# Optimization experiments

Measured on AMD Instinct MI355X. Metric: run time of the kernel, lower is better.

## Reference

```python
import jax, jax.numpy as jnp
import numpy as np
import math

B, N = 1, 512
C_S, C_Z, C_H, H, PQ, PV = 384, 128, 16, 12, 4, 8
INF, EPS = 100000.0, 1e-8


def setup_inputs() -> dict:
    key = jax.random.key(0)
    ks = jax.random.split(key, 16)
    sc = 0.02
    return {
        "s": jax.random.normal(ks[0], (B, N, C_S), jnp.float32),
        "z": jax.random.normal(ks[1], (B, N, N, C_Z), jnp.float32),
        "t_trans": jax.random.normal(ks[2], (B, N, 3), jnp.float32),
        "t_rots": jax.random.normal(ks[3], (B, N, 3, 3), jnp.float32),
        "mask": jnp.ones((B, N), jnp.float32),
        "Wq": jax.random.normal(ks[4], (C_S, H * C_H), jnp.float32) * sc,
        "bq": jnp.zeros((H * C_H,), jnp.float32),
        "Wkv": jax.random.normal(ks[5], (C_S, 2 * H * C_H), jnp.float32) * sc,
        "bkv": jnp.zeros((2 * H * C_H,), jnp.float32),
        "Wqp": jax.random.normal(ks[6], (C_S, H * PQ * 3), jnp.float32) * sc,
        "bqp": jnp.zeros((H * PQ * 3,), jnp.float32),
        "Wkvp": jax.random.normal(ks[7], (C_S, H * (PQ + PV) * 3), jnp.float32) * sc,
        "bkvp": jnp.zeros((H * (PQ + PV) * 3,), jnp.float32),
        "Wb": jax.random.normal(ks[8], (C_Z, H), jnp.float32) * sc,
        "bb": jnp.zeros((H,), jnp.float32),
        "head_weights": jnp.full((H,), 0.5413, jnp.float32),  # softplus^-1(1) init
        "Wout": jax.random.normal(ks[9], (H * (C_Z + C_H + PV * 4), C_S), jnp.float32) * sc,
        "bout": jnp.zeros((C_S,), jnp.float32),
    }


def _split3_stack(x):
    # torch.split into 3 chunks along -1, then stack on new last axis -> [..., P, 3]
    return jnp.stack(jnp.split(x, 3, axis=-1), axis=-1)


def reference(s, z, t_trans, t_rots, mask, Wq, bq, Wkv, bkv, Wqp, bqp, Wkvp, bkvp,
              Wb, bb, head_weights, Wout, bout):
    q = (s @ Wq + bq).reshape(B, N, H, C_H)
    kv = (s @ Wkv + bkv).reshape(B, N, H, 2 * C_H)
    k, v = kv[..., :C_H], kv[..., C_H:]

    # point projections, moved to global frame: r @ p + t
    qp = _split3_stack(s @ Wqp + bqp)                      # [B,N,H*PQ,3] local
    qp = jnp.einsum('bnij,bnpj->bnpi', t_rots, qp) + t_trans[:, :, None, :]
    q_pts = qp.reshape(B, N, H, PQ, 3)
    kvp = _split3_stack(s @ Wkvp + bkvp)                   # [B,N,H*(PQ+PV),3]
    kvp = jnp.einsum('bnij,bnpj->bnpi', t_rots, kvp) + t_trans[:, :, None, :]
    kvp = kvp.reshape(B, N, H, PQ + PV, 3)
    k_pts, v_pts = kvp[..., :PQ, :], kvp[..., PQ:, :]

    b = z @ Wb + bb                                        # [B,N,N,H]

    a = jnp.einsum('bihc,bjhc->bhij', q, k) * math.sqrt(1.0 / (3 * C_H))
    a = a + math.sqrt(1.0 / 3) * jnp.transpose(b, (0, 3, 1, 2))

    # point-distance attention: [B,N,N,H,PQ]
    d2 = jnp.sum((q_pts[:, :, None] - k_pts[:, None]) ** 2, axis=-1)
    hw = jax.nn.softplus(head_weights) * math.sqrt(1.0 / (3 * (PQ * 9.0 / 2)))
    a = a + (-0.5) * jnp.einsum('bijhp,h->bhij', d2, hw)

    square_mask = INF * (mask[:, :, None] * mask[:, None, :] - 1.0)  # [B,N,N]
    a = jax.nn.softmax(a + square_mask[:, None], axis=-1)  # [B,H,N,N]

    o = jnp.einsum('bhij,bjhc->bihc', a, v).reshape(B, N, H * C_H)

    o_pt = jnp.einsum('bhij,bjhpx->bihpx', a, v_pts)       # [B,N,H,PV,3] global
    # invert frame: r^T @ (p - t)
    o_pt = jnp.einsum('bnji,bnhpj->bnhpi', t_rots, o_pt - t_trans[:, :, None, None, :])
    o_pt_norm = jnp.sqrt(jnp.sum(o_pt ** 2, axis=-1) + EPS).reshape(B, N, H * PV)
    o_pt = o_pt.reshape(B, N, H * PV, 3)

    o_pair = jnp.einsum('bhij,bijc->bihc', a, z).reshape(B, N, H * C_Z)

    cat = jnp.concatenate(
        [o, o_pt[..., 0], o_pt[..., 1], o_pt[..., 2], o_pt_norm, o_pair], axis=-1)
    return cat @ Wout + bout
```

## Files before the change

kernel.cpp:

```cpp
#include <hip/hip_runtime.h>
#include <math.h>

#define N 512
#define CS 384
#define CZ 128
#define CH 16
#define NH 12
#define PQ 4
#define PV 8

#define OFF_Q     0
#define OFF_K     98304
#define OFF_V     196608
#define OFF_QRAW  294912
#define OFF_KVRAW 368640
#define OFF_QPTS  589824
#define OFF_KPTS  663552
#define OFF_VPTS  737280
#define OFF_A     884736
#define OFF_CAT   4030464

__global__ __launch_bounds__(128) void proj_kernel(
    const float* __restrict__ s,
    const float* __restrict__ Wq,  const float* __restrict__ bq,
    const float* __restrict__ Wkv, const float* __restrict__ bkv,
    const float* __restrict__ Wqp, const float* __restrict__ bqp,
    const float* __restrict__ Wkvp,const float* __restrict__ bkvp,
    float* __restrict__ ws)
{
    __shared__ float st[16 * CS];
    const int n0 = blockIdx.x * 16;
    for (int idx = threadIdx.x * 4; idx < 16 * CS; idx += 128 * 4)
        *(float4*)&st[idx] = *(const float4*)&s[n0 * CS + idx];
    __syncthreads();

    const int tc = threadIdx.x & 31;
    const int tr = threadIdx.x >> 5;
    const int u0 = blockIdx.y * 128 + tc * 4;
    const int r0 = tr * 4;

    const float* W; const float* bptr; int ncol, lc0;
    if (u0 < 192)      { W = Wq;   bptr = bq;   ncol = 192; lc0 = u0; }
    else if (u0 < 576) { W = Wkv;  bptr = bkv;  ncol = 384; lc0 = u0 - 192; }
    else if (u0 < 720) { W = Wqp;  bptr = bqp;  ncol = 144; lc0 = u0 - 576; }
    else               { W = Wkvp; bptr = bkvp; ncol = 432; lc0 = u0 - 720; }

    float acc[4][4];
    #pragma unroll
    for (int r = 0; r < 4; r++)
        #pragma unroll
        for (int c = 0; c < 4; c++) acc[r][c] = 0.f;

    for (int k = 0; k < CS; k += 4) {
        float4 w0 = *(const float4*)&W[(k + 0) * ncol + lc0];
        float4 w1 = *(const float4*)&W[(k + 1) * ncol + lc0];
        float4 w2 = *(const float4*)&W[(k + 2) * ncol + lc0];
        float4 w3 = *(const float4*)&W[(k + 3) * ncol + lc0];
        #pragma unroll
        for (int r = 0; r < 4; r++) {
            float4 sv = *(const float4*)&st[(r0 + r) * CS + k];
            acc[r][0] += sv.x * w0.x + sv.y * w1.x + sv.z * w2.x + sv.w * w3.x;
            acc[r][1] += sv.x * w0.y + sv.y * w1.y + sv.z * w2.y + sv.w * w3.y;
            acc[r][2] += sv.x * w0.z + sv.y * w1.z + sv.z * w2.z + sv.w * w3.z;
            acc[r][3] += sv.x * w0.w + sv.y * w1.w + sv.z * w2.w + sv.w * w3.w;
        }
    }

    #pragma unroll
    for (int c = 0; c < 4; c++) {
        const int u = u0 + c;
        const float bias = bptr[lc0 + c];
        #pragma unroll
        for (int r = 0; r < 4; r++) {
            const int n = n0 + r0 + r;
            int oidx;
            if (u < 192) oidx = OFF_Q + n * 192 + u;
            else if (u < 576) {
                int lc = u - 192, h = lc >> 5, w = lc & 31;
                oidx = (w < 16) ? OFF_K + n * 192 + h * 16 + w
                                : OFF_V + n * 192 + h * 16 + (w - 16);
            } else if (u < 720) oidx = OFF_QRAW + n * 144 + (u - 576);
            else                oidx = OFF_KVRAW + n * 432 + (u - 720);
            ws[oidx] = acc[r][c] + bias;
        }
    }
}

__global__ __launch_bounds__(192) void point_kernel(
    const float* __restrict__ t_trans, const float* __restrict__ t_rots,
    float* __restrict__ ws)
{
    const int n = blockIdx.x;
    const int t = threadIdx.x;
    __shared__ float R[9], tr[3];
    if (t < 9) R[t] = t_rots[n * 9 + t];
    if (t < 3) tr[t] = t_trans[n * 3 + t];
    __syncthreads();

    float x0, x1, x2;
    int base;
    if (t < 48) {
        int idx = t;
        x0 = ws[OFF_QRAW + n * 144 + 0 * 48 + idx];
        x1 = ws[OFF_QRAW + n * 144 + 1 * 48 + idx];
        x2 = ws[OFF_QRAW + n * 144 + 2 * 48 + idx];
        int h = idx >> 2, p = idx & 3;
        base = OFF_QPTS + ((n * NH + h) * PQ + p) * 3;
    } else {
        int idx = t - 48;
        x0 = ws[OFF_KVRAW + n * 432 + 0 * 144 + idx];
        x1 = ws[OFF_KVRAW + n * 432 + 1 * 144 + idx];
        x2 = ws[OFF_KVRAW + n * 432 + 2 * 144 + idx];
        int h = idx / 12, p = idx % 12;
        if (p < PQ) base = OFF_KPTS + ((n * NH + h) * PQ + p) * 3;
        else        base = OFF_VPTS + ((n * NH + h) * PV + (p - PQ)) * 3;
    }
    ws[base + 0] = R[0] * x0 + R[1] * x1 + R[2] * x2 + tr[0];
    ws[base + 1] = R[3] * x0 + R[4] * x1 + R[5] * x2 + tr[1];
    ws[base + 2] = R[6] * x0 + R[7] * x1 + R[8] * x2 + tr[2];
}

__global__ __launch_bounds__(192) void logitA_kernel(
    const float* __restrict__ mask, const float* __restrict__ hweights,
    float* __restrict__ ws)
{
    const int j0 = blockIdx.x * 16;
    const int i0 = blockIdx.y * 16;
    const int t = threadIdx.x;

    __shared__ float qt[16 * 200];
    __shared__ float kt[16 * 200];
    __shared__ float qpt[16 * 148];
    __shared__ float kpt[16 * 148];
    __shared__ float mi[16], mj[16];

    {
        const float* src = ws + OFF_Q + i0 * 192;
        for (int idx = t * 4; idx < 3072; idx += 768) {
            float4 v = *(const float4*)&src[idx];
            *(float4*)&qt[(idx / 192) * 200 + idx % 192] = v;
        }
    }
    {
        const float* src = ws + OFF_K + j0 * 192;
        for (int idx = t * 4; idx < 3072; idx += 768) {
            float4 v = *(const float4*)&src[idx];
            *(float4*)&kt[(idx / 192) * 200 + idx % 192] = v;
        }
    }
    {
        const float* src = ws + OFF_QPTS + i0 * 144;
        for (int idx = t * 4; idx < 2304; idx += 768) {
            float4 v = *(const float4*)&src[idx];
            *(float4*)&qpt[(idx / 144) * 148 + idx % 144] = v;
        }
    }
    {
        const float* src = ws + OFF_KPTS + j0 * 144;
        for (int idx = t * 4; idx < 2304; idx += 768) {
            float4 v = *(const float4*)&src[idx];
            *(float4*)&kpt[(idx / 144) * 148 + idx % 144] = v;
        }
    }
    if (t < 16) { mi[t] = mask[i0 + t]; mj[t] = mask[j0 + t]; }
    __syncthreads();

    const int jj = t & 15;
    const int h = t >> 4;
    const float hw = log1pf(expf(hweights[h])) * 0.13608276348795434f;
    const float cqk = 0.14433756729740643f;

    float4 kr0 = *(const float4*)&kt[jj * 200 + h * 16 + 0];
    float4 kr1 = *(const float4*)&kt[jj * 200 + h * 16 + 4];
    float4 kr2 = *(const float4*)&kt[jj * 200 + h * 16 + 8];
    float4 kr3 = *(const float4*)&kt[jj * 200 + h * 16 + 12];
    float4 kp0 = *(const float4*)&kpt[jj * 148 + h * 12 + 0];
    float4 kp1 = *(const float4*)&kpt[jj * 148 + h * 12 + 4];
    float4 kp2 = *(const float4*)&kpt[jj * 148 + h * 12 + 8];
    const float mjv = mj[jj];

    for (int ii = 0; ii < 16; ii++) {
        float4 q0 = *(const float4*)&qt[ii * 200 + h * 16 + 0];
        float4 q1 = *(const float4*)&qt[ii * 200 + h * 16 + 4];
        float4 q2 = *(const float4*)&qt[ii * 200 + h * 16 + 8];
        float4 q3 = *(const float4*)&qt[ii * 200 + h * 16 + 12];
        float qk = q0.x * kr0.x + q0.y * kr0.y + q0.z * kr0.z + q0.w * kr0.w
                 + q1.x * kr1.x + q1.y * kr1.y + q1.z * kr1.z + q1.w * kr1.w
                 + q2.x * kr2.x + q2.y * kr2.y + q2.z * kr2.z + q2.w * kr2.w
                 + q3.x * kr3.x + q3.y * kr3.y + q3.z * kr3.z + q3.w * kr3.w;
        float4 p0 = *(const float4*)&qpt[ii * 148 + h * 12 + 0];
        float4 p1 = *(const float4*)&qpt[ii * 148 + h * 12 + 4];
        float4 p2 = *(const float4*)&qpt[ii * 148 + h * 12 + 8];
        float e, d2 = 0.f;
        e = p0.x - kp0.x; d2 += e * e;  e = p0.y - kp0.y; d2 += e * e;
        e = p0.z - kp0.z; d2 += e * e;  e = p0.w - kp0.w; d2 += e * e;
        e = p1.x - kp1.x; d2 += e * e;  e = p1.y - kp1.y; d2 += e * e;
        e = p1.z - kp1.z; d2 += e * e;  e = p1.w - kp1.w; d2 += e * e;
        e = p2.x - kp2.x; d2 += e * e;  e = p2.y - kp2.y; d2 += e * e;
        e = p2.z - kp2.z; d2 += e * e;  e = p2.w - kp2.w; d2 += e * e;
        float sm = 100000.0f * (mi[ii] * mjv - 1.0f);
        ws[OFF_A + ((size_t)(i0 + ii) * NH + h) * N + j0 + jj] =
            qk * cqk - 0.5f * hw * d2 + sm;
    }
}

__global__ __launch_bounds__(512) void bsoft_kernel(
    const float* __restrict__ z, const float* __restrict__ Wb,
    const float* __restrict__ bb, float* __restrict__ ws)
{
    const int i = blockIdx.x;
    const int t = threadIdx.x;
    __shared__ float zt[128 * 132];
    __shared__ float wbt[12 * 132];
    __shared__ float wred[8][4];

    for (int idx = t; idx < CZ * NH; idx += 512) {
        int c = idx / NH, h = idx % NH;
        wbt[h * 132 + c] = Wb[idx];
    }

    const int jj = t & 127;
    const int hg = t >> 7;
    const int h0 = hg * 3;
    const float bb0 = bb[h0], bb1 = bb[h0 + 1], bb2 = bb[h0 + 2];
    const float cb = 0.5773502691896258f;

    float lg[3][4];

    for (int T = 0; T < 4; T++) {
        __syncthreads();
        const float* zsrc = z + ((size_t)i * N + T * 128) * CZ;
        for (int idx = t * 4; idx < 16384; idx += 2048) {
            float4 v = *(const float4*)&zsrc[idx];
            *(float4*)&zt[(idx >> 7) * 132 + (idx & 127)] = v;
        }
        __syncthreads();

        float a0 = bb0, a1 = bb1, a2 = bb2;
        const float* zr = &zt[jj * 132];
        const float* w0 = &wbt[(h0 + 0) * 132];
        const float* w1 = &wbt[(h0 + 1) * 132];
        const float* w2 = &wbt[(h0 + 2) * 132];
        #pragma unroll
        for (int c = 0; c < CZ; c += 4) {
            float4 zq = *(const float4*)&zr[c];
            float4 q0 = *(const float4*)&w0[c];
            float4 q1 = *(const float4*)&w1[c];
            float4 q2 = *(const float4*)&w2[c];
            a0 += zq.x * q0.x + zq.y * q0.y + zq.z * q0.z + zq.w * q0.w;
            a1 += zq.x * q1.x + zq.y * q1.y + zq.z * q1.z + zq.w * q1.w;
            a2 += zq.x * q2.x + zq.y * q2.y + zq.z * q2.z + zq.w * q2.w;
        }
        const float* arow = ws + OFF_A + (size_t)i * NH * N + T * 128 + jj;
        lg[0][T] = arow[(size_t)(h0 + 0) * N] + cb * a0;
        lg[1][T] = arow[(size_t)(h0 + 1) * N] + cb * a1;
        lg[2][T] = arow[(size_t)(h0 + 2) * N] + cb * a2;
    }

    const int wv = t >> 6;
    float mx[3], sm[3];
    #pragma unroll
    for (int r = 0; r < 3; r++) {
        float m = fmaxf(fmaxf(lg[r][0], lg[r][1]), fmaxf(lg[r][2], lg[r][3]));
        #pragma unroll
        for (int o = 32; o > 0; o >>= 1) m = fmaxf(m, __shfl_xor(m, o));
        mx[r] = m;
    }
    if ((t & 63) == 0) {
        wred[wv][0] = mx[0]; wred[wv][1] = mx[1]; wred[wv][2] = mx[2];
    }
    __syncthreads();
    #pragma unroll
    for (int r = 0; r < 3; r++)
        mx[r] = fmaxf(wred[hg * 2][r], wred[hg * 2 + 1][r]);
    __syncthreads();
    #pragma unroll
    for (int r = 0; r < 3; r++) {
        float s = 0.f;
        #pragma unroll
        for (int T = 0; T < 4; T++) { lg[r][T] = __expf(lg[r][T] - mx[r]); s += lg[r][T]; }
        #pragma unroll
        for (int o = 32; o > 0; o >>= 1) s += __shfl_xor(s, o);
        sm[r] = s;
    }
    if ((t & 63) == 0) {
        wred[wv][0] = sm[0]; wred[wv][1] = sm[1]; wred[wv][2] = sm[2];
    }
    __syncthreads();
    #pragma unroll
    for (int r = 0; r < 3; r++) {
        float inv = 1.0f / (wred[hg * 2][r] + wred[hg * 2 + 1][r]);
        float* prow = ws + OFF_A + ((size_t)i * NH + h0 + r) * N + jj;
        #pragma unroll
        for (int T = 0; T < 4; T++)
            prow[T * 128] = lg[r][T] * inv;
    }
}

__global__ __launch_bounds__(832) void finish_kernel(
    const float* __restrict__ z, const float* __restrict__ t_trans,
    const float* __restrict__ t_rots, const float* __restrict__ ws_c,
    float* __restrict__ ws)
{
    const int i = blockIdx.x;
    const int t = threadIdx.x;
    __shared__ float a_s[12 * 520];

    {
        const float* src = ws_c + OFF_A + (size_t)i * (NH * N);
        for (int idx = t * 4; idx < NH * N; idx += 832 * 4) {
            float4 v = *(const float4*)&src[idx];
            int h = idx >> 9, j = idx & 511;
            *(float4*)&a_s[h * 520 + j] = v;
        }
    }
    __syncthreads();

    float* cat = ws + OFF_CAT + (size_t)i * 2112;

    if (t < 512) {
        const int c = t & 127, hg = t >> 7;
        const float* zrow = z + (size_t)i * N * CZ + c;
        const float* a0 = a_s + (hg + 0) * 520;
        const float* a1 = a_s + (hg + 4) * 520;
        const float* a2 = a_s + (hg + 8) * 520;
        float acc0 = 0.f, acc1 = 0.f, acc2 = 0.f;
        #pragma unroll 8
        for (int j = 0; j < N; j++) {
            float zv = zrow[(size_t)j * CZ];
            acc0 += a0[j] * zv; acc1 += a1[j] * zv; acc2 += a2[j] * zv;
        }
        cat[576 + (hg + 0) * CZ + c] = acc0;
        cat[576 + (hg + 4) * CZ + c] = acc1;
        cat[576 + (hg + 8) * CZ + c] = acc2;
    } else if (t < 704) {
        const int u = t - 512, h = u >> 4, cc = u & 15;
        const float* vcol = ws_c + OFF_V + h * 16 + cc;
        const float* ah = a_s + h * 520;
        float acc = 0.f;
        #pragma unroll 8
        for (int j = 0; j < N; j++)
            acc += ah[j] * vcol[j * 192];
        cat[h * 16 + cc] = acc;
    } else if (t < 800) {
        const int u = t - 704, h = u >> 3, p = u & 7;
        const float* vp = ws_c + OFF_VPTS + (h * PV + p) * 3;
        const float* ah = a_s + h * 520;
        float g0 = 0.f, g1 = 0.f, g2 = 0.f;
        #pragma unroll 4
        for (int j = 0; j < N; j++) {
            float av = ah[j];
            const float* vpj = vp + j * (NH * PV * 3);
            g0 += av * vpj[0]; g1 += av * vpj[1]; g2 += av * vpj[2];
        }
        float R[9], ti[3];
        #pragma unroll
        for (int x = 0; x < 9; x++) R[x] = t_rots[i * 9 + x];
        #pragma unroll
        for (int x = 0; x < 3; x++) ti[x] = t_trans[i * 3 + x];
        g0 -= ti[0]; g1 -= ti[1]; g2 -= ti[2];
        float l0 = R[0] * g0 + R[3] * g1 + R[6] * g2;
        float l1 = R[1] * g0 + R[4] * g1 + R[7] * g2;
        float l2 = R[2] * g0 + R[5] * g1 + R[8] * g2;
        float nrm = sqrtf(l0 * l0 + l1 * l1 + l2 * l2 + 1e-8f);
        int e = h * PV + p;
        cat[192 + e] = l0;
        cat[288 + e] = l1;
        cat[384 + e] = l2;
        cat[480 + e] = nrm;
    }
}

__global__ __launch_bounds__(384) void init_out_kernel(
    const float* __restrict__ bout, float* __restrict__ out)
{
    out[(size_t)blockIdx.x * 384 + threadIdx.x] = bout[threadIdx.x];
}

__global__ __launch_bounds__(384) void out_kernel(
    const float* __restrict__ Wout, const float* __restrict__ ws,
    float* __restrict__ out)
{
    const int rt = blockIdx.x;
    const int kc = blockIdx.y;
    const int t = threadIdx.x;
    __shared__ float ct[16 * 264];
    for (int idx = t * 4; idx < 16 * 264; idx += 384 * 4) {
        int rr = idx / 264, kk = idx % 264;
        *(float4*)&ct[idx] =
            *(const float4*)&ws[OFF_CAT + (size_t)(rt * 16 + rr) * 2112 + kc * 264 + kk];
    }
    __syncthreads();
    const int cq = t % 96, rg = t / 96;
    const int c0 = cq * 4;
    float acc[4][4] = {};
    const float* Wp = Wout + (size_t)kc * 264 * 384 + c0;
    for (int kk = 0; kk < 264; kk++) {
        float4 w = *(const float4*)&Wp[(size_t)kk * 384];
        #pragma unroll
        for (int r = 0; r < 4; r++) {
            float sv = ct[(rg * 4 + r) * 264 + kk];
            acc[r][0] += sv * w.x; acc[r][1] += sv * w.y;
            acc[r][2] += sv * w.z; acc[r][3] += sv * w.w;
        }
    }
    #pragma unroll
    for (int r = 0; r < 4; r++) {
        float* op = out + (size_t)(rt * 16 + rg * 4 + r) * 384 + c0;
        atomicAdd(&op[0], acc[r][0]);
        atomicAdd(&op[1], acc[r][1]);
        atomicAdd(&op[2], acc[r][2]);
        atomicAdd(&op[3], acc[r][3]);
    }
}

extern "C" void kernel_launch(void* const* d_in, const int* in_sizes, int n_in,
                              void* d_out, int out_size, void* d_ws, size_t ws_size,
                              hipStream_t stream) {
    const float* s       = (const float*)d_in[0];
    const float* z       = (const float*)d_in[1];
    const float* t_trans = (const float*)d_in[2];
    const float* t_rots  = (const float*)d_in[3];
    const float* mask    = (const float*)d_in[4];
    const float* Wq      = (const float*)d_in[5];
    const float* bq      = (const float*)d_in[6];
    const float* Wkv     = (const float*)d_in[7];
    const float* bkv     = (const float*)d_in[8];
    const float* Wqp     = (const float*)d_in[9];
    const float* bqp     = (const float*)d_in[10];
    const float* Wkvp    = (const float*)d_in[11];
    const float* bkvp    = (const float*)d_in[12];
    const float* Wb      = (const float*)d_in[13];
    const float* bb      = (const float*)d_in[14];
    const float* hweights= (const float*)d_in[15];
    const float* Wout    = (const float*)d_in[16];
    const float* bout    = (const float*)d_in[17];
    float* ws  = (float*)d_ws;
    float* out = (float*)d_out;

    init_out_kernel<<<512, 384, 0, stream>>>(bout, out);
    proj_kernel<<<dim3(32, 9), 128, 0, stream>>>(s, Wq, bq, Wkv, bkv, Wqp, bqp, Wkvp, bkvp, ws);
    point_kernel<<<512, 192, 0, stream>>>(t_trans, t_rots, ws);
    logitA_kernel<<<dim3(32, 32), 192, 0, stream>>>(mask, hweights, ws);
    bsoft_kernel<<<512, 512, 0, stream>>>(z, Wb, bb, ws);
    finish_kernel<<<512, 832, 0, stream>>>(z, t_trans, t_rots, ws, ws);
    out_kernel<<<dim3(32, 8), 384, 0, stream>>>(Wout, ws, out);
}
```

Measured before the change: 427.5 us.

## Retile finish, bsoft, proj and out kernels with vectorized loads and planar v-points

Several kernels change at once. finish_kernel drops from 832 to 384 threads: each thread now computes a float4 of channels for two heads in the z pair reduction, and the o and point reductions use float4 loads over j. v_pts is stored as planar x/y/z arrays indexed by position so the point reduction can read it contiguously. bsoft reads Wb through scalar, wave-uniform loads instead of staging it in shared memory, proj_kernel doubles its thread count with fewer rows per thread, and out_kernel unrolls k by 4 with float4 shared-memory reads. The aim is fewer scalar loads and better memory coalescing, at the cost of more registers per thread and a __syncthreads inside the j loop of finish_kernel.

```diff
diff --git a/kernel.cpp b/kernel.cpp
--- a/kernel.cpp
+++ b/kernel.cpp
@@ -17,10 +17,11 @@
 #define OFF_QPTS  589824
 #define OFF_KPTS  663552
 #define OFF_VPTS  737280
+#define VPLANE    49152
 #define OFF_A     884736
 #define OFF_CAT   4030464
 
-__global__ __launch_bounds__(128) void proj_kernel(
+__global__ __launch_bounds__(256) void proj_kernel(
     const float* __restrict__ s,
     const float* __restrict__ Wq,  const float* __restrict__ bq,
     const float* __restrict__ Wkv, const float* __restrict__ bkv,
@@ -30,14 +31,14 @@
 {
     __shared__ float st[16 * CS];
     const int n0 = blockIdx.x * 16;
-    for (int idx = threadIdx.x * 4; idx < 16 * CS; idx += 128 * 4)
+    for (int idx = threadIdx.x * 4; idx < 16 * CS; idx += 256 * 4)
         *(float4*)&st[idx] = *(const float4*)&s[n0 * CS + idx];
     __syncthreads();
 
     const int tc = threadIdx.x & 31;
     const int tr = threadIdx.x >> 5;
     const int u0 = blockIdx.y * 128 + tc * 4;
-    const int r0 = tr * 4;
+    const int r0 = tr * 2;
 
     const float* W; const float* bptr; int ncol, lc0;
     if (u0 < 192)      { W = Wq;   bptr = bq;   ncol = 192; lc0 = u0; }
@@ -45,9 +46,9 @@
     else if (u0 < 720) { W = Wqp;  bptr = bqp;  ncol = 144; lc0 = u0 - 576; }
     else               { W = Wkvp; bptr = bkvp; ncol = 432; lc0 = u0 - 720; }
 
-    float acc[4][4];
-    #pragma unroll
-    for (int r = 0; r < 4; r++)
+    float acc[2][4];
+    #pragma unroll
+    for (int r = 0; r < 2; r++)
         #pragma unroll
         for (int c = 0; c < 4; c++) acc[r][c] = 0.f;
 
@@ -57,7 +58,7 @@
         float4 w2 = *(const float4*)&W[(k + 2) * ncol + lc0];
         float4 w3 = *(const float4*)&W[(k + 3) * ncol + lc0];
         #pragma unroll
-        for (int r = 0; r < 4; r++) {
+        for (int r = 0; r < 2; r++) {
             float4 sv = *(const float4*)&st[(r0 + r) * CS + k];
             acc[r][0] += sv.x * w0.x + sv.y * w1.x + sv.z * w2.x + sv.w * w3.x;
             acc[r][1] += sv.x * w0.y + sv.y * w1.y + sv.z * w2.y + sv.w * w3.y;
@@ -71,7 +72,7 @@
         const int u = u0 + c;
         const float bias = bptr[lc0 + c];
         #pragma unroll
-        for (int r = 0; r < 4; r++) {
+        for (int r = 0; r < 2; r++) {
             const int n = n0 + r0 + r;
             int oidx;
             if (u < 192) oidx = OFF_Q + n * 192 + u;
@@ -98,26 +99,34 @@
     __syncthreads();
 
     float x0, x1, x2;
-    int base;
     if (t < 48) {
         int idx = t;
         x0 = ws[OFF_QRAW + n * 144 + 0 * 48 + idx];
         x1 = ws[OFF_QRAW + n * 144 + 1 * 48 + idx];
         x2 = ws[OFF_QRAW + n * 144 + 2 * 48 + idx];
         int h = idx >> 2, p = idx & 3;
-        base = OFF_QPTS + ((n * NH + h) * PQ + p) * 3;
+        int base = OFF_QPTS + ((n * NH + h) * PQ + p) * 3;
+        ws[base + 0] = R[0] * x0 + R[1] * x1 + R[2] * x2 + tr[0];
+        ws[base + 1] = R[3] * x0 + R[4] * x1 + R[5] * x2 + tr[1];
+        ws[base + 2] = R[6] * x0 + R[7] * x1 + R[8] * x2 + tr[2];
     } else {
         int idx = t - 48;
         x0 = ws[OFF_KVRAW + n * 432 + 0 * 144 + idx];
         x1 = ws[OFF_KVRAW + n * 432 + 1 * 144 + idx];
         x2 = ws[OFF_KVRAW + n * 432 + 2 * 144 + idx];
         int h = idx / 12, p = idx % 12;
-        if (p < PQ) base = OFF_KPTS + ((n * NH + h) * PQ + p) * 3;
-        else        base = OFF_VPTS + ((n * NH + h) * PV + (p - PQ)) * 3;
-    }
-    ws[base + 0] = R[0] * x0 + R[1] * x1 + R[2] * x2 + tr[0];
-    ws[base + 1] = R[3] * x0 + R[4] * x1 + R[5] * x2 + tr[1];
-    ws[base + 2] = R[6] * x0 + R[7] * x1 + R[8] * x2 + tr[2];
+        if (p < PQ) {
+            int base = OFF_KPTS + ((n * NH + h) * PQ + p) * 3;
+            ws[base + 0] = R[0] * x0 + R[1] * x1 + R[2] * x2 + tr[0];
+            ws[base + 1] = R[3] * x0 + R[4] * x1 + R[5] * x2 + tr[1];
+            ws[base + 2] = R[6] * x0 + R[7] * x1 + R[8] * x2 + tr[2];
+        } else {
+            int hp = h * PV + (p - PQ);
+            ws[OFF_VPTS + 0 * VPLANE + hp * N + n] = R[0] * x0 + R[1] * x1 + R[2] * x2 + tr[0];
+            ws[OFF_VPTS + 1 * VPLANE + hp * N + n] = R[3] * x0 + R[4] * x1 + R[5] * x2 + tr[1];
+            ws[OFF_VPTS + 2 * VPLANE + hp * N + n] = R[6] * x0 + R[7] * x1 + R[8] * x2 + tr[2];
+        }
+    }
 }
 
 __global__ __launch_bounds__(192) void logitA_kernel(
@@ -211,19 +220,14 @@
     const int i = blockIdx.x;
     const int t = threadIdx.x;
     __shared__ float zt[128 * 132];
-    __shared__ float wbt[12 * 132];
     __shared__ float wred[8][4];
 
-    for (int idx = t; idx < CZ * NH; idx += 512) {
-        int c = idx / NH, h = idx % NH;
-        wbt[h * 132 + c] = Wb[idx];
-    }
-
     const int jj = t & 127;
-    const int hg = t >> 7;
-    const int h0 = hg * 3;
+    const int hgu = __builtin_amdgcn_readfirstlane(t >> 7);
+    const int h0 = hgu * 3;
     const float bb0 = bb[h0], bb1 = bb[h0 + 1], bb2 = bb[h0 + 2];
     const float cb = 0.5773502691896258f;
+    const float* __restrict__ Wp = Wb + h0;
 
     float lg[3][4];
 
@@ -238,18 +242,15 @@
 
         float a0 = bb0, a1 = bb1, a2 = bb2;
         const float* zr = &zt[jj * 132];
-        const float* w0 = &wbt[(h0 + 0) * 132];
-        const float* w1 = &wbt[(h0 + 1) * 132];
-        const float* w2 = &wbt[(h0 + 2) * 132];
         #pragma unroll
         for (int c = 0; c < CZ; c += 4) {
             float4 zq = *(const float4*)&zr[c];
-            float4 q0 = *(const float4*)&w0[c];
-            float4 q1 = *(const float4*)&w1[c];
-            float4 q2 = *(const float4*)&w2[c];
-            a0 += zq.x * q0.x + zq.y * q0.y + zq.z * q0.z + zq.w * q0.w;
-            a1 += zq.x * q1.x + zq.y * q1.y + zq.z * q1.z + zq.w * q1.w;
-            a2 += zq.x * q2.x + zq.y * q2.y + zq.z * q2.z + zq.w * q2.w;
+            a0 += zq.x * Wp[(c + 0) * NH]     + zq.y * Wp[(c + 1) * NH]
+                + zq.z * Wp[(c + 2) * NH]     + zq.w * Wp[(c + 3) * NH];
+            a1 += zq.x * Wp[(c + 0) * NH + 1] + zq.y * Wp[(c + 1) * NH + 1]
+                + zq.z * Wp[(c + 2) * NH + 1] + zq.w * Wp[(c + 3) * NH + 1];
+            a2 += zq.x * Wp[(c + 0) * NH + 2] + zq.y * Wp[(c + 1) * NH + 2]
+                + zq.z * Wp[(c + 2) * NH + 2] + zq.w * Wp[(c + 3) * NH + 2];
         }
         const float* arow = ws + OFF_A + (size_t)i * NH * N + T * 128 + jj;
         lg[0][T] = arow[(size_t)(h0 + 0) * N] + cb * a0;
@@ -272,7 +273,7 @@
     __syncthreads();
     #pragma unroll
     for (int r = 0; r < 3; r++)
-        mx[r] = fmaxf(wred[hg * 2][r], wred[hg * 2 + 1][r]);
+        mx[r] = fmaxf(wred[hgu * 2][r], wred[hgu * 2 + 1][r]);
     __syncthreads();
     #pragma unroll
     for (int r = 0; r < 3; r++) {
@@ -289,7 +290,7 @@
     __syncthreads();
     #pragma unroll
     for (int r = 0; r < 3; r++) {
-        float inv = 1.0f / (wred[hg * 2][r] + wred[hg * 2 + 1][r]);
+        float inv = 1.0f / (wred[hgu * 2][r] + wred[hgu * 2 + 1][r]);
         float* prow = ws + OFF_A + ((size_t)i * NH + h0 + r) * N + jj;
         #pragma unroll
         for (int T = 0; T < 4; T++)
@@ -297,7 +298,7 @@
     }
 }
 
-__global__ __launch_bounds__(832) void finish_kernel(
+__global__ __launch_bounds__(384) void finish_kernel(
     const float* __restrict__ z, const float* __restrict__ t_trans,
     const float* __restrict__ t_rots, const float* __restrict__ ws_c,
     float* __restrict__ ws)
@@ -308,7 +309,7 @@
 
     {
         const float* src = ws_c + OFF_A + (size_t)i * (NH * N);
-        for (int idx = t * 4; idx < NH * N; idx += 832 * 4) {
+        for (int idx = t * 4; idx < NH * N; idx += 384 * 4) {
             float4 v = *(const float4*)&src[idx];
             int h = idx >> 9, j = idx & 511;
             *(float4*)&a_s[h * 520 + j] = v;
@@ -318,41 +319,82 @@
 
     float* cat = ws + OFF_CAT + (size_t)i * 2112;
 
-    if (t < 512) {
-        const int c = t & 127, hg = t >> 7;
-        const float* zrow = z + (size_t)i * N * CZ + c;
-        const float* a0 = a_s + (hg + 0) * 520;
-        const float* a1 = a_s + (hg + 4) * 520;
-        const float* a2 = a_s + (hg + 8) * 520;
-        float acc0 = 0.f, acc1 = 0.f, acc2 = 0.f;
-        #pragma unroll 8
-        for (int j = 0; j < N; j++) {
-            float zv = zrow[(size_t)j * CZ];
-            acc0 += a0[j] * zv; acc1 += a1[j] * zv; acc2 += a2[j] * zv;
-        }
-        cat[576 + (hg + 0) * CZ + c] = acc0;
-        cat[576 + (hg + 4) * CZ + c] = acc1;
-        cat[576 + (hg + 8) * CZ + c] = acc2;
-    } else if (t < 704) {
-        const int u = t - 512, h = u >> 4, cc = u & 15;
-        const float* vcol = ws_c + OFF_V + h * 16 + cc;
-        const float* ah = a_s + h * 520;
-        float acc = 0.f;
-        #pragma unroll 8
-        for (int j = 0; j < N; j++)
-            acc += ah[j] * vcol[j * 192];
-        cat[h * 16 + cc] = acc;
-    } else if (t < 800) {
-        const int u = t - 704, h = u >> 3, p = u & 7;
-        const float* vp = ws_c + OFF_VPTS + (h * PV + p) * 3;
-        const float* ah = a_s + h * 520;
-        float g0 = 0.f, g1 = 0.f, g2 = 0.f;
-        #pragma unroll 4
-        for (int j = 0; j < N; j++) {
-            float av = ah[j];
-            const float* vpj = vp + j * (NH * PV * 3);
-            g0 += av * vpj[0]; g1 += av * vpj[1]; g2 += av * vpj[2];
-        }
+    float4 accA = {0,0,0,0}, accB = {0,0,0,0};
+    float4 accO = {0,0,0,0};
+    float g0 = 0.f, g1 = 0.f, g2 = 0.f;
+
+    const int cg = t & 31;
+    const int hp6 = t >> 5;
+    const float* zb = z + (size_t)i * N * CZ + cg * 4;
+    const float* ahA = a_s + hp6 * 520;
+    const float* ahB = a_s + (hp6 + 6) * 520;
+
+    const int uo = t - 192;
+    const int ho = uo >> 2, cgo = uo & 3;
+    const float* ahO = a_s + ho * 520;
+
+    const int up = t - 240;
+    const float* ahP = a_s + (up >> 3) * 520;
+    const float* vx = ws_c + OFF_VPTS + 0 * VPLANE + up * N;
+    const float* vy = ws_c + OFF_VPTS + 1 * VPLANE + up * N;
+    const float* vz = ws_c + OFF_VPTS + 2 * VPLANE + up * N;
+
+    for (int jt = 0; jt < N; jt += 64) {
+        if (t < 192) {
+            #pragma unroll 4
+            for (int jo = 0; jo < 64; jo += 4) {
+                const int j = jt + jo;
+                float4 aA = *(const float4*)&ahA[j];
+                float4 aB = *(const float4*)&ahB[j];
+                float4 z0 = *(const float4*)&zb[(size_t)(j + 0) * CZ];
+                float4 z1 = *(const float4*)&zb[(size_t)(j + 1) * CZ];
+                float4 z2 = *(const float4*)&zb[(size_t)(j + 2) * CZ];
+                float4 z3 = *(const float4*)&zb[(size_t)(j + 3) * CZ];
+                accA.x += aA.x * z0.x + aA.y * z1.x + aA.z * z2.x + aA.w * z3.x;
+                accA.y += aA.x * z0.y + aA.y * z1.y + aA.z * z2.y + aA.w * z3.y;
+                accA.z += aA.x * z0.z + aA.y * z1.z + aA.z * z2.z + aA.w * z3.z;
+                accA.w += aA.x * z0.w + aA.y * z1.w + aA.z * z2.w + aA.w * z3.w;
+                accB.x += aB.x * z0.x + aB.y * z1.x + aB.z * z2.x + aB.w * z3.x;
+                accB.y += aB.x * z0.y + aB.y * z1.y + aB.z * z2.y + aB.w * z3.y;
+                accB.z += aB.x * z0.z + aB.y * z1.z + aB.z * z2.z + aB.w * z3.z;
+                accB.w += aB.x * z0.w + aB.y * z1.w + aB.z * z2.w + aB.w * z3.w;
+            }
+        } else if (t < 240) {
+            #pragma unroll 4
+            for (int jo = 0; jo < 64; jo += 4) {
+                const int j = jt + jo;
+                float4 a4 = *(const float4*)&ahO[j];
+                float4 v0 = *(const float4*)&ws_c[OFF_V + (j + 0) * 192 + ho * 16 + cgo * 4];
+                float4 v1 = *(const float4*)&ws_c[OFF_V + (j + 1) * 192 + ho * 16 + cgo * 4];
+                float4 v2 = *(const float4*)&ws_c[OFF_V + (j + 2) * 192 + ho * 16 + cgo * 4];
+                float4 v3 = *(const float4*)&ws_c[OFF_V + (j + 3) * 192 + ho * 16 + cgo * 4];
+                accO.x += a4.x * v0.x + a4.y * v1.x + a4.z * v2.x + a4.w * v3.x;
+                accO.y += a4.x * v0.y + a4.y * v1.y + a4.z * v2.y + a4.w * v3.y;
+                accO.z += a4.x * v0.z + a4.y * v1.z + a4.z * v2.z + a4.w * v3.z;
+                accO.w += a4.x * v0.w + a4.y * v1.w + a4.z * v2.w + a4.w * v3.w;
+            }
+        } else if (t < 336) {
+            #pragma unroll 4
+            for (int jo = 0; jo < 64; jo += 4) {
+                const int j = jt + jo;
+                float4 a4 = *(const float4*)&ahP[j];
+                float4 x4 = *(const float4*)&vx[j];
+                float4 y4 = *(const float4*)&vy[j];
+                float4 z4 = *(const float4*)&vz[j];
+                g0 += a4.x * x4.x + a4.y * x4.y + a4.z * x4.z + a4.w * x4.w;
+                g1 += a4.x * y4.x + a4.y * y4.y + a4.z * y4.z + a4.w * y4.w;
+                g2 += a4.x * z4.x + a4.y * z4.y + a4.z * z4.z + a4.w * z4.w;
+            }
+        }
+        __syncthreads();
+    }
+
+    if (t < 192) {
+        *(float4*)&cat[576 + hp6 * CZ + cg * 4]       = accA;
+        *(float4*)&cat[576 + (hp6 + 6) * CZ + cg * 4] = accB;
+    } else if (t < 240) {
+        *(float4*)&cat[ho * 16 + cgo * 4] = accO;
+    } else if (t < 336) {
         float R[9], ti[3];
         #pragma unroll
         for (int x = 0; x < 9; x++) R[x] = t_rots[i * 9 + x];
@@ -363,11 +405,10 @@
         float l1 = R[1] * g0 + R[4] * g1 + R[7] * g2;
         float l2 = R[2] * g0 + R[5] * g1 + R[8] * g2;
         float nrm = sqrtf(l0 * l0 + l1 * l1 + l2 * l2 + 1e-8f);
-        int e = h * PV + p;
-        cat[192 + e] = l0;
-        cat[288 + e] = l1;
-        cat[384 + e] = l2;
-        cat[480 + e] = nrm;
+        cat[192 + up] = l0;
+        cat[288 + up] = l1;
+        cat[384 + up] = l2;
+        cat[480 + up] = nrm;
     }
 }
 
@@ -395,13 +436,18 @@
     const int c0 = cq * 4;
     float acc[4][4] = {};
     const float* Wp = Wout + (size_t)kc * 264 * 384 + c0;
-    for (int kk = 0; kk < 264; kk++) {
-        float4 w = *(const float4*)&Wp[(size_t)kk * 384];
+    for (int kk = 0; kk < 264; kk += 4) {
+        float4 w0 = *(const float4*)&Wp[(size_t)(kk + 0) * 384];
+        float4 w1 = *(const float4*)&Wp[(size_t)(kk + 1) * 384];
+        float4 w2 = *(const float4*)&Wp[(size_t)(kk + 2) * 384];
+        float4 w3 = *(const float4*)&Wp[(size_t)(kk + 3) * 384];
         #pragma unroll
         for (int r = 0; r < 4; r++) {
-            float sv = ct[(rg * 4 + r) * 264 + kk];
-            acc[r][0] += sv * w.x; acc[r][1] += sv * w.y;
-            acc[r][2] += sv * w.z; acc[r][3] += sv * w.w;
+            float4 sv = *(const float4*)&ct[(rg * 4 + r) * 264 + kk];
+            acc[r][0] += sv.x * w0.x + sv.y * w1.x + sv.z * w2.x + sv.w * w3.x;
+            acc[r][1] += sv.x * w0.y + sv.y * w1.y + sv.z * w2.y + sv.w * w3.y;
+            acc[r][2] += sv.x * w0.z + sv.y * w1.z + sv.z * w2.z + sv.w * w3.z;
+            acc[r][3] += sv.x * w0.w + sv.y * w1.w + sv.z * w2.w + sv.w * w3.w;
         }
     }
     #pragma unroll
@@ -439,10 +485,10 @@
     float* out = (float*)d_out;
 
     init_out_kernel<<<512, 384, 0, stream>>>(bout, out);
-    proj_kernel<<<dim3(32, 9), 128, 0, stream>>>(s, Wq, bq, Wkv, bkv, Wqp, bqp, Wkvp, bkvp, ws);
+    proj_kernel<<<dim3(32, 9), 256, 0, stream>>>(s, Wq, bq, Wkv, bkv, Wqp, bqp, Wkvp, bkvp, ws);
     point_kernel<<<512, 192, 0, stream>>>(t_trans, t_rots, ws);
     logitA_kernel<<<dim3(32, 32), 192, 0, stream>>>(mask, hweights, ws);
     bsoft_kernel<<<512, 512, 0, stream>>>(z, Wb, bb, ws);
-    finish_kernel<<<512, 832, 0, stream>>>(z, t_trans, t_rots, ws, ws);
+    finish_kernel<<<512, 384, 0, stream>>>(z, t_trans, t_rots, ws, ws);
     out_kernel<<<dim3(32, 8), 384, 0, stream>>>(Wout, ws, out);
 }
```

New measurement: 553.9 us. 1.3x slower.
